# Optimization experiments

Measured on AMD Instinct MI355X. Metric: run time of the kernel, lower is better.

## Reference

```python
import jax, jax.numpy as jnp
import numpy as np

D = 15            # tree depth; leaves at level 0, root at level D
INPUT_DIM = 64
MEM_DIM = 256     # must equal 4*INPUT_DIM (h-update mixes rr with x)
HID_DIM = 128


def _lin(key, fi, fo):
    kw, kb = jax.random.split(key)
    w = jax.random.normal(kw, (fi, fo), jnp.float32) / np.sqrt(fi)
    b = jax.random.normal(kb, (fo,), jnp.float32) * 0.01
    return w, b


def setup_inputs() -> dict:
    key = jax.random.key(0)
    N = 2 ** (D + 1) - 1          # 65535 nodes (complete binary tree, heap order)
    I = 2 ** D - 1                # internal nodes
    depth = np.floor(np.log2(np.arange(1, N + 1))).astype(np.int64)  # depth of node i
    node_order_np = D - depth     # leaves -> 0, root -> D
    parents = np.repeat(np.arange(I, dtype=np.int64), 2)   # sorted, consecutive per parent
    children = np.arange(1, N, dtype=np.int64)             # heap children 2i+1, 2i+2
    adjacency_list = jnp.asarray(np.stack([parents, children], axis=1))
    edge_order = jnp.asarray(node_order_np[parents])
    ks = jax.random.split(key, 24)
    inp = {
        'oper_feat': jax.random.uniform(ks[0], (N, 4), jnp.float32),
        'tb_feat': jax.random.uniform(ks[1], (N, 11), jnp.float32),
        'filter_feat': jax.random.uniform(ks[2], (N, 18), jnp.float32),
        'join_feat': jax.random.uniform(ks[3], (N, 37), jnp.float32),
        'c_a': jax.random.normal(ks[4], (N, MEM_DIM), jnp.float32) * 0.1,
        'c_b': jax.random.normal(ks[5], (N, 5 * INPUT_DIM), jnp.float32) * 0.1,
    }
    inp['w_op1'], inp['b_op1'] = _lin(ks[6], 4, INPUT_DIM)
    inp['w_op2'], inp['b_op2'] = _lin(ks[7], INPUT_DIM, INPUT_DIM)
    inp['w_tb1'], inp['b_tb1'] = _lin(ks[8], 11, INPUT_DIM)
    inp['w_tb2'], inp['b_tb2'] = _lin(ks[9], INPUT_DIM, INPUT_DIM)
    inp['w_ft1'], inp['b_ft1'] = _lin(ks[10], 18, INPUT_DIM)
    inp['w_ft2'], inp['b_ft2'] = _lin(ks[11], INPUT_DIM, INPUT_DIM)
    inp['w_jn1'], inp['b_jn1'] = _lin(ks[12], 37, INPUT_DIM)
    inp['w_jn2'], inp['b_jn2'] = _lin(ks[13], INPUT_DIM, INPUT_DIM)
    inp['w_xou'], inp['b_xou'] = _lin(ks[14], 4 * INPUT_DIM, 3 * MEM_DIM)
    inp['w_ab'], inp['b_ab'] = _lin(ks[15], MEM_DIM, MEM_DIM)
    inp['w_btoa'], inp['b_btoa'] = _lin(ks[16], 5 * INPUT_DIM, MEM_DIM)
    inp['w_ca'], inp['b_ca'] = _lin(ks[17], 4 * INPUT_DIM, MEM_DIM)
    inp['w_cb'], inp['b_cb'] = _lin(ks[18], 4 * INPUT_DIM, MEM_DIM)
    inp['w_o1'], inp['b_o1'] = _lin(ks[19], MEM_DIM, HID_DIM)
    inp['w_o2'], inp['b_o2'] = _lin(ks[20], HID_DIM, 1)
    inp['node_order'] = jnp.asarray(node_order_np)
    inp['adjacency_list'] = adjacency_list
    inp['edge_order'] = edge_order
    inp['feed'] = 0
    return inp


def _mlp2(f, w1, b1, w2, b2):
    return jax.nn.relu(jax.nn.relu(f @ w1 + b1) @ w2 + b2)


def reference(oper_feat, tb_feat, filter_feat, join_feat, c_a, c_b,
              w_op1, b_op1, w_op2, b_op2, w_tb1, b_tb1, w_tb2, b_tb2,
              w_ft1, b_ft1, w_ft2, b_ft2, w_jn1, b_jn1, w_jn2, b_jn2,
              w_xou, b_xou, w_ab, b_ab, w_btoa, b_btoa, w_ca, b_ca,
              w_cb, b_cb, w_o1, b_o1, w_o2, b_o2,
              node_order, adjacency_list, edge_order, feed):
    N = node_order.shape[0]
    op = _mlp2(oper_feat, w_op1, b_op1, w_op2, b_op2)
    tb = _mlp2(tb_feat, w_tb1, b_tb1, w_tb2, b_tb2)
    ft = _mlp2(filter_feat, w_ft1, b_ft1, w_ft2, b_ft2)
    jn = _mlp2(join_feat, w_jn1, b_jn1, w_jn2, b_jn2)
    x = jnp.concatenate([op, tb, ft, jn], axis=1)        # [N, 4*input_dim] == [N, mem_dim]
    xou = x @ w_xou + b_xou                               # [N, 3*mem_dim]
    xx, ff, rr = jnp.split(xou, 3, axis=1)
    ff = jax.nn.sigmoid(ff)
    rr = jax.nn.sigmoid(rr)
    cb = c_b @ w_btoa + b_btoa                            # con_mpl_btoa (no activation)
    wa = jax.nn.sigmoid(c_a @ w_ca + b_ca)
    wb = jax.nn.sigmoid(cb @ w_cb + b_cb)
    c_ab = jax.nn.relu((wa * c_a + wb * cb) @ w_ab + b_ab)
    c = jnp.zeros((N, MEM_DIM), x.dtype)
    h = jnp.zeros((N, MEM_DIM), x.dtype)
    c = jnp.where((node_order == 0)[:, None], c_a, c)
    c = jnp.where((node_order == feed)[:, None], c_ab, c)
    par = adjacency_list[:, 0]
    chi = adjacency_list[:, 1]
    L = int(node_order.max())
    for n in range(feed + 1, L + 1):
        em = (edge_order == n).astype(x.dtype)[:, None]
        # segment-sum children cell states into their parents (level-n edges only)
        c_sum = jax.ops.segment_sum(c[chi] * em, par, num_segments=N)
        nm = (node_order == n)[:, None]
        c = jnp.where(nm, ff * c_sum + (1.0 - ff) * xx, c)
        h = jnp.where(nm, rr * jnp.tanh(c) + (1.0 - rr) * x, h)
    hid = jax.nn.relu(h @ w_o1 + b_o1)
    return jax.nn.sigmoid(hid @ w_o2 + b_o2)              # [N, 1]
```

## Files before the change

### kernel.cpp

```cpp
#include <hip/hip_runtime.h>
#include <cstdint>

#define I_NODES 32767
#define N_NODES 65535
#define NLEAF   32768

typedef float f32x4 __attribute__((ext_vector_type(4)));
typedef short bf16x8 __attribute__((ext_vector_type(8)));
typedef int   i32x4 __attribute__((ext_vector_type(4)));

__device__ __forceinline__ float sigmoidf_(float v) {
    return 1.0f / (1.0f + __expf(-v));
}
__device__ __forceinline__ float tanhf_(float v) {
    return 1.0f - 2.0f / (1.0f + __expf(2.0f * v));
}
__device__ __forceinline__ short f2bf(float f) {
    union { float f; unsigned u; } v; v.f = f;
    unsigned r = (v.u + 0x7FFF + ((v.u >> 16) & 1)) >> 16;
    return (short)r;
}
__device__ __forceinline__ float bf2f(short b) {
    union { float f; unsigned u; } v; v.u = ((unsigned)(unsigned short)b) << 16;
    return v.f;
}

__global__ __launch_bounds__(256) void prep_weights(
    const float* __restrict__ w_xou, const float* __restrict__ w_btoa,
    const float* __restrict__ w_ca,  const float* __restrict__ w_cb,
    const float* __restrict__ w_ab,  const float* __restrict__ w_o1,
    const float* __restrict__ w_op1, const float* __restrict__ w_tb1,
    const float* __restrict__ w_ft1, const float* __restrict__ w_jn1,
    const float* __restrict__ w_op2, const float* __restrict__ w_tb2,
    const float* __restrict__ w_ft2, const float* __restrict__ w_jn2,
    const float* __restrict__ b_op1, const float* __restrict__ b_tb1,
    const float* __restrict__ b_ft1, const float* __restrict__ b_jn1,
    const float* __restrict__ b_op2, const float* __restrict__ b_tb2,
    const float* __restrict__ b_ft2, const float* __restrict__ b_jn2,
    short* __restrict__ wT_xou, short* __restrict__ wT_btoa,
    short* __restrict__ wT_ca,  short* __restrict__ wT_cb,
    short* __restrict__ wT_ab,  short* __restrict__ wT_o1,
    short* __restrict__ W1T,    short* __restrict__ W2T,
    float* __restrict__ b1cat,  float* __restrict__ b2cat)
{
    int r = blockIdx.x * 256 + threadIdx.x;
    if (r < 196608) { wT_xou[r] = f2bf(w_xou[(size_t)(r % 256) * 768 + r / 256]); return; }
    r -= 196608;
    if (r < 81920)  { wT_btoa[r] = f2bf(w_btoa[(size_t)(r % 320) * 256 + r / 320]); return; }
    r -= 81920;
    if (r < 65536)  { wT_ca[r] = f2bf(w_ca[(size_t)(r % 256) * 256 + r / 256]); return; }
    r -= 65536;
    if (r < 65536)  { wT_cb[r] = f2bf(w_cb[(size_t)(r % 256) * 256 + r / 256]); return; }
    r -= 65536;
    if (r < 65536)  { wT_ab[r] = f2bf(w_ab[(size_t)(r % 256) * 256 + r / 256]); return; }
    r -= 65536;
    if (r < 32768)  { wT_o1[r] = f2bf(w_o1[(size_t)(r % 256) * 128 + r / 256]); return; }
    r -= 32768;
    if (r < 24576) {
        int j = r / 96, k = r % 96;
        int s = j >> 6, jj = j & 63;
        int off = (s == 0) ? 0 : (s == 1) ? 4 : (s == 2) ? 15 : 33;
        int Ks  = (s == 0) ? 4 : (s == 1) ? 11 : (s == 2) ? 18 : 37;
        const float* w = (s == 0) ? w_op1 : (s == 1) ? w_tb1 : (s == 2) ? w_ft1 : w_jn1;
        W1T[r] = (k >= off && k < off + Ks) ? f2bf(w[(k - off) * 64 + jj]) : (short)0;
        return;
    }
    r -= 24576;
    if (r < 65536) {
        int j = r >> 8, k = r & 255;
        int s = j >> 6, jj = j & 63;
        const float* w = (s == 0) ? w_op2 : (s == 1) ? w_tb2 : (s == 2) ? w_ft2 : w_jn2;
        W2T[r] = ((k >> 6) == s) ? f2bf(w[(k & 63) * 64 + jj]) : (short)0;
        return;
    }
    r -= 65536;
    if (r < 256) {
        int s = r >> 6, jj = r & 63;
        b1cat[r] = (s == 0) ? b_op1[jj] : (s == 1) ? b_tb1[jj] : (s == 2) ? b_ft1[jj] : b_jn1[jj];
        return;
    }
    r -= 256;
    if (r < 256) {
        int s = r >> 6, jj = r & 63;
        b2cat[r] = (s == 0) ? b_op2[jj] : (s == 1) ? b_tb2[jj] : (s == 2) ? b_ft2[jj] : b_jn2[jj];
    }
}

__global__ __launch_bounds__(256) void pack_feat(
    const float* __restrict__ oper, const float* __restrict__ tbf,
    const float* __restrict__ ftf,  const float* __restrict__ jnf,
    short* __restrict__ xfeat)
{
    int idx = blockIdx.x * 256 + threadIdx.x;
    int node = idx / 96, f = idx - node * 96;
    float v = 0.0f;
    if (node < I_NODES) {
        if (f < 4)       v = oper[node * 4 + f];
        else if (f < 15) v = tbf[node * 11 + (f - 4)];
        else if (f < 33) v = ftf[node * 18 + (f - 15)];
        else if (f < 70) v = jnf[node * 37 + (f - 33)];
    }
    xfeat[idx] = f2bf(v);
}

__global__ __launch_bounds__(256) void conv_leaf_kernel(
    const float* __restrict__ c_a, const float* __restrict__ c_b,
    short* __restrict__ ca_o, short* __restrict__ cb_o)
{
    size_t i = (size_t)blockIdx.x * 256 + threadIdx.x;
    if (i < (size_t)NLEAF * 256) ca_o[i] = f2bf(c_a[(size_t)I_NODES * 256 + i]);
    if (i < (size_t)NLEAF * 320) cb_o[i] = f2bf(c_b[(size_t)I_NODES * 320 + i]);
}

template <int ACT, int MODE>
__global__ __launch_bounds__(256) void gemm_mfma(
    const short* __restrict__ A, const short* __restrict__ Bt,
    const float* __restrict__ bias,
    float* __restrict__ fout0, const float* __restrict__ caf,
    float* __restrict__ fout1, float* __restrict__ fout2,
    short* __restrict__ bout,
    const short* __restrict__ e1, const short* __restrict__ e2,
    int M, int K, int Nn)
{
    __shared__ short Asl[128 * 40];
    __shared__ short Bsl[128 * 40];

    const int tid = threadIdx.x;
    const int bm = blockIdx.x * 128;
    const int bn = blockIdx.y * 128;
    const int wave = tid >> 6, lane = tid & 63;
    const int m = lane & 15, q = lane >> 4;
    const int rw = (wave & 1) * 64, cw = (wave >> 1) * 64;

    f32x4 acc[4][4] = {};

    for (int k0 = 0; k0 < K; k0 += 32) {
#pragma unroll
        for (int i = 0; i < 2; i++) {
            int id = tid + i * 256;
            int row = id >> 2, ch = id & 3;
            i32x4 va = *(const i32x4*)(A + (size_t)(bm + row) * K + k0 + ch * 8);
            *(i32x4*)&Asl[row * 40 + ch * 8] = va;
            i32x4 vb = *(const i32x4*)(Bt + (size_t)(bn + row) * K + k0 + ch * 8);
            *(i32x4*)&Bsl[row * 40 + ch * 8] = vb;
        }
        __syncthreads();

        bf16x8 bfrag[4];
#pragma unroll
        for (int ct = 0; ct < 4; ct++)
            bfrag[ct] = *(const bf16x8*)&Bsl[(cw + ct * 16 + m) * 40 + q * 8];
#pragma unroll
        for (int rt = 0; rt < 4; rt++) {
            bf16x8 afrag = *(const bf16x8*)&Asl[(rw + rt * 16 + m) * 40 + q * 8];
#pragma unroll
            for (int ct = 0; ct < 4; ct++)
                acc[rt][ct] = __builtin_amdgcn_mfma_f32_16x16x32_bf16(
                    afrag, bfrag[ct], acc[rt][ct], 0, 0, 0);
        }
        __syncthreads();
    }

#pragma unroll
    for (int rt = 0; rt < 4; rt++) {
#pragma unroll
        for (int ct = 0; ct < 4; ct++) {
            int col = bn + cw + ct * 16 + m;
            float bv = bias[col];
#pragma unroll
            for (int r = 0; r < 4; r++) {
                int row = bm + rw + rt * 16 + q * 4 + r;
                float v = acc[rt][ct][r] + bv;
                if (MODE == 0) {
                    if (ACT == 1) v = fmaxf(v, 0.0f);
                    else if (ACT == 2) v = sigmoidf_(v);
                    fout0[(size_t)row * Nn + col] = v;
                } else if (MODE == 1) {
                    int seg = col >> 8, cc = col & 255;
                    if (seg == 0)      fout0[(size_t)row * 256 + cc] = v;
                    else if (seg == 1) fout1[(size_t)row * 256 + cc] = sigmoidf_(v);
                    else               fout2[(size_t)row * 256 + cc] = sigmoidf_(v);
                } else if (MODE == 2) {
                    if (ACT == 1) v = fmaxf(v, 0.0f);
                    else if (ACT == 2) v = sigmoidf_(v);
                    bout[(size_t)row * Nn + col] = f2bf(v);
                } else {
                    size_t idx = (size_t)row * 256 + col;
                    float t = bf2f(e1[idx]) * caf[idx] + sigmoidf_(v) * bf2f(e2[idx]);
                    bout[idx] = f2bf(t);
                }
            }
        }
    }
}

__global__ __launch_bounds__(256) void level_kernel(
    float* __restrict__ c, const float* __restrict__ ff,
    const float* __restrict__ xx, const float* __restrict__ rr,
    const short* __restrict__ x, short* __restrict__ h,
    int start)
{
    size_t idx = (size_t)blockIdx.x * 256 + threadIdx.x;
    int p = start + (int)(idx >> 8);
    int j = (int)(idx & 255);
    size_t pr = (size_t)p * 256 + j;
    float cs = c[(size_t)(2 * p + 1) * 256 + j] + c[(size_t)(2 * p + 2) * 256 + j];
    float f = ff[pr];
    float cv = f * cs + (1.0f - f) * xx[pr];
    c[pr] = cv;
    float r = rr[pr];
    h[pr] = f2bf(r * tanhf_(cv) + (1.0f - r) * bf2f(x[pr]));
}

__global__ __launch_bounds__(1024) void small_levels_kernel(
    float* __restrict__ c, const float* __restrict__ ff,
    const float* __restrict__ xx, const float* __restrict__ rr,
    const short* __restrict__ x, short* __restrict__ h)
{
    const int tid = threadIdx.x;
    for (int n = 8; n <= 15; n++) {
        int d = 15 - n;
        int start = (1 << d) - 1;
        int total = (1 << d) * 256;
        for (int idx = tid; idx < total; idx += 1024) {
            int p = start + (idx >> 8);
            int j = idx & 255;
            size_t pr = (size_t)p * 256 + j;
            float cs = c[(size_t)(2 * p + 1) * 256 + j] + c[(size_t)(2 * p + 2) * 256 + j];
            float f = ff[pr];
            float cv = f * cs + (1.0f - f) * xx[pr];
            c[pr] = cv;
            float r = rr[pr];
            h[pr] = f2bf(r * tanhf_(cv) + (1.0f - r) * bf2f(x[pr]));
        }
        __syncthreads();
    }
}

__global__ __launch_bounds__(256) void out2_kernel(
    const short* __restrict__ hid, const float* __restrict__ w_o2,
    const float* __restrict__ b_o2, const float* __restrict__ b_o1,
    float* __restrict__ out)
{
    int wave = threadIdx.x >> 6;
    int lane = threadIdx.x & 63;
    int node = blockIdx.x * 4 + wave;
    if (node >= N_NODES) return;
    float h0, h1;
    if (node < I_NODES) {
        const short* hrow = hid + (size_t)node * 128;
        h0 = bf2f(hrow[lane]); h1 = bf2f(hrow[lane + 64]);
    } else {
        h0 = fmaxf(b_o1[lane], 0.0f); h1 = fmaxf(b_o1[lane + 64], 0.0f);
    }
    float p = h0 * w_o2[lane] + h1 * w_o2[lane + 64];
#pragma unroll
    for (int off = 32; off > 0; off >>= 1) p += __shfl_xor(p, off);
    if (lane == 0) out[node] = sigmoidf_(p + b_o2[0]);
}

extern "C" void kernel_launch(void* const* d_in, const int* in_sizes, int n_in,
                              void* d_out, int out_size, void* d_ws, size_t ws_size,
                              hipStream_t stream)
{
    const float* oper  = (const float*)d_in[0];
    const float* tbf   = (const float*)d_in[1];
    const float* ftf   = (const float*)d_in[2];
    const float* jnf   = (const float*)d_in[3];
    const float* c_a   = (const float*)d_in[4];
    const float* c_b   = (const float*)d_in[5];
    const float* w_op1 = (const float*)d_in[6],  *b_op1 = (const float*)d_in[7];
    const float* w_op2 = (const float*)d_in[8],  *b_op2 = (const float*)d_in[9];
    const float* w_tb1 = (const float*)d_in[10], *b_tb1 = (const float*)d_in[11];
    const float* w_tb2 = (const float*)d_in[12], *b_tb2 = (const float*)d_in[13];
    const float* w_ft1 = (const float*)d_in[14], *b_ft1 = (const float*)d_in[15];
    const float* w_ft2 = (const float*)d_in[16], *b_ft2 = (const float*)d_in[17];
    const float* w_jn1 = (const float*)d_in[18], *b_jn1 = (const float*)d_in[19];
    const float* w_jn2 = (const float*)d_in[20], *b_jn2 = (const float*)d_in[21];
    const float* w_xou = (const float*)d_in[22], *b_xou = (const float*)d_in[23];
    const float* w_ab  = (const float*)d_in[24], *b_ab  = (const float*)d_in[25];
    const float* w_btoa= (const float*)d_in[26], *b_btoa= (const float*)d_in[27];
    const float* w_ca  = (const float*)d_in[28], *b_ca  = (const float*)d_in[29];
    const float* w_cb  = (const float*)d_in[30], *b_cb  = (const float*)d_in[31];
    const float* w_o1  = (const float*)d_in[32], *b_o1  = (const float*)d_in[33];
    const float* w_o2  = (const float*)d_in[34], *b_o2  = (const float*)d_in[35];

    char* WS = (char*)d_ws;
    short* wT_xou  = (short*)WS;
    short* wT_btoa = wT_xou  + 196608;
    short* wT_ca   = wT_btoa + 81920;
    short* wT_cb   = wT_ca   + 65536;
    short* wT_ab   = wT_cb   + 65536;
    short* wT_o1   = wT_ab   + 65536;
    short* W1T     = wT_o1   + 32768;
    short* W2T     = W1T     + 24576;
    float* b1cat   = (float*)(W2T + 65536);
    float* b2cat   = b1cat + 256;
    const size_t MB = 1 << 20;
    const size_t OFF_XF   = 2 * MB;
    const size_t OFF_HE   = OFF_XF   + (size_t)32768 * 96 * 2;
    const size_t OFF_X    = OFF_HE   + (size_t)32768 * 256 * 2;
    const size_t OFF_XX   = OFF_X    + (size_t)32768 * 256 * 2;
    const size_t OFF_FF   = OFF_XX   + (size_t)32768 * 256 * 4;
    const size_t OFF_RR   = OFF_FF   + (size_t)32768 * 256 * 4;
    const size_t OFF_C    = OFF_RR   + (size_t)32768 * 256 * 4;
    const size_t OFF_CA   = OFF_C    + (size_t)65536 * 256 * 4;
    const size_t OFF_CBIN = OFF_CA   + (size_t)32768 * 256 * 2;
    const size_t OFF_CB   = OFF_CBIN + (size_t)32768 * 320 * 2;
    const size_t OFF_WA   = OFF_CB   + (size_t)32768 * 256 * 2;

    short* xfeat = (short*)(WS + OFF_XF);
    short* henc  = (short*)(WS + OFF_HE);
    short* x     = (short*)(WS + OFF_X);
    float* xx    = (float*)(WS + OFF_XX);
    float* ff    = (float*)(WS + OFF_FF);
    float* rr    = (float*)(WS + OFF_RR);
    float* c     = (float*)(WS + OFF_C);
    short* cal   = (short*)(WS + OFF_CA);
    short* cbin  = (short*)(WS + OFF_CBIN);
    short* cb    = (short*)(WS + OFF_CB);
    short* wa    = (short*)(WS + OFF_WA);
    short* h     = (short*)(WS + OFF_CA);
    short* hid   = (short*)(WS + OFF_CB);
    float* out   = (float*)d_out;
    const float* caf = c_a + (size_t)I_NODES * 256;

    prep_weights<<<(598528 + 255) / 256, 256, 0, stream>>>(
        w_xou, w_btoa, w_ca, w_cb, w_ab, w_o1,
        w_op1, w_tb1, w_ft1, w_jn1, w_op2, w_tb2, w_ft2, w_jn2,
        b_op1, b_tb1, b_ft1, b_jn1, b_op2, b_tb2, b_ft2, b_jn2,
        wT_xou, wT_btoa, wT_ca, wT_cb, wT_ab, wT_o1, W1T, W2T, b1cat, b2cat);
    pack_feat<<<(32768 * 96) / 256, 256, 0, stream>>>(oper, tbf, ftf, jnf, xfeat);
    conv_leaf_kernel<<<(NLEAF * 320 + 255) / 256, 256, 0, stream>>>(c_a, c_b, cal, cbin);

    gemm_mfma<1, 2><<<dim3(256, 2), 256, 0, stream>>>(
        xfeat, W1T, b1cat, nullptr, nullptr, nullptr, nullptr, henc, nullptr, nullptr,
        32768, 96, 256);
    gemm_mfma<1, 2><<<dim3(256, 2), 256, 0, stream>>>(
        henc, W2T, b2cat, nullptr, nullptr, nullptr, nullptr, x, nullptr, nullptr,
        32768, 256, 256);

    gemm_mfma<0, 1><<<dim3(256, 6), 256, 0, stream>>>(
        x, wT_xou, b_xou, xx, nullptr, ff, rr, nullptr, nullptr, nullptr,
        32768, 256, 768);

    gemm_mfma<0, 2><<<dim3(256, 2), 256, 0, stream>>>(
        cbin, wT_btoa, b_btoa, nullptr, nullptr, nullptr, nullptr, cb, nullptr, nullptr,
        32768, 320, 256);
    gemm_mfma<2, 2><<<dim3(256, 2), 256, 0, stream>>>(
        cal, wT_ca, b_ca, nullptr, nullptr, nullptr, nullptr, wa, nullptr, nullptr,
        32768, 256, 256);
    gemm_mfma<0, 3><<<dim3(256, 2), 256, 0, stream>>>(
        cb, wT_cb, b_cb, nullptr, caf, nullptr, nullptr, wa , wa, cb,
        32768, 256, 256);
    gemm_mfma<1, 0><<<dim3(256, 2), 256, 0, stream>>>(
        wa, wT_ab, b_ab, c + (size_t)I_NODES * 256, nullptr, nullptr, nullptr,
        nullptr, nullptr, nullptr, 32768, 256, 256);

    for (int n = 1; n <= 7; n++) {
        int d = 15 - n;
        int start = (1 << d) - 1;
        int count = 1 << d;
        level_kernel<<<count, 256, 0, stream>>>(c, ff, xx, rr, x, h, start);
    }
    small_levels_kernel<<<1, 1024, 0, stream>>>(c, ff, xx, rr, x, h);

    gemm_mfma<1, 2><<<dim3(256, 1), 256, 0, stream>>>(
        h, wT_o1, b_o1, nullptr, nullptr, nullptr, nullptr, hid, nullptr, nullptr,
        32768, 256, 128);
    out2_kernel<<<(N_NODES + 3) / 4, 256, 0, stream>>>(hid, w_o2, b_o2, b_o1, out);
}
```

Baseline: 510.9 us.

## Fuse prep kernels, convert leaf inputs in GEMM, persistent level kernel with grid barrier

Merges the weight prep, feature packing and leaf output computation into one launch. The leaf c_a/c_b bf16 conversion pass is removed: the GEMM now reads fp32 directly and converts while loading tiles, and the btoa and ca GEMMs share a single launch. The 15 tree levels run in one persistent kernel of 256 blocks synchronised by an atomic grid barrier, and the final MLP layer is folded into the o1 GEMM epilogue, so the hid buffer and out2 kernel disappear. This cuts launch count and intermediate traffic. The cost is a spin barrier that relies on all 256 blocks being co-resident, and small levels now spread across many blocks with a barrier between each.

```diff
diff --git a/kernel.cpp b/kernel.cpp
--- a/kernel.cpp
+++ b/kernel.cpp
@@ -25,7 +25,7 @@
     return v.f;
 }
 
-__global__ __launch_bounds__(256) void prep_weights(
+__global__ __launch_bounds__(256) void prep_all(
     const float* __restrict__ w_xou, const float* __restrict__ w_btoa,
     const float* __restrict__ w_ca,  const float* __restrict__ w_cb,
     const float* __restrict__ w_ab,  const float* __restrict__ w_o1,
@@ -37,11 +37,17 @@
     const float* __restrict__ b_ft1, const float* __restrict__ b_jn1,
     const float* __restrict__ b_op2, const float* __restrict__ b_tb2,
     const float* __restrict__ b_ft2, const float* __restrict__ b_jn2,
+    const float* __restrict__ oper,  const float* __restrict__ tbf,
+    const float* __restrict__ ftf,   const float* __restrict__ jnf,
+    const float* __restrict__ b_o1,  const float* __restrict__ w_o2,
+    const float* __restrict__ b_o2,
     short* __restrict__ wT_xou, short* __restrict__ wT_btoa,
     short* __restrict__ wT_ca,  short* __restrict__ wT_cb,
     short* __restrict__ wT_ab,  short* __restrict__ wT_o1,
     short* __restrict__ W1T,    short* __restrict__ W2T,
-    float* __restrict__ b1cat,  float* __restrict__ b2cat)
+    float* __restrict__ b1cat,  float* __restrict__ b2cat,
+    short* __restrict__ xfeat,  float* __restrict__ outv,
+    int* __restrict__ bar)
 {
     int r = blockIdx.x * 256 + threadIdx.x;
     if (r < 196608) { wT_xou[r] = f2bf(w_xou[(size_t)(r % 256) * 768 + r / 256]); return; }
@@ -83,48 +89,45 @@
     if (r < 256) {
         int s = r >> 6, jj = r & 63;
         b2cat[r] = (s == 0) ? b_op2[jj] : (s == 1) ? b_tb2[jj] : (s == 2) ? b_ft2[jj] : b_jn2[jj];
-    }
-}
-
-__global__ __launch_bounds__(256) void pack_feat(
-    const float* __restrict__ oper, const float* __restrict__ tbf,
-    const float* __restrict__ ftf,  const float* __restrict__ jnf,
-    short* __restrict__ xfeat)
-{
-    int idx = blockIdx.x * 256 + threadIdx.x;
-    int node = idx / 96, f = idx - node * 96;
-    float v = 0.0f;
-    if (node < I_NODES) {
-        if (f < 4)       v = oper[node * 4 + f];
-        else if (f < 15) v = tbf[node * 11 + (f - 4)];
-        else if (f < 33) v = ftf[node * 18 + (f - 15)];
-        else if (f < 70) v = jnf[node * 37 + (f - 33)];
-    }
-    xfeat[idx] = f2bf(v);
-}
-
-__global__ __launch_bounds__(256) void conv_leaf_kernel(
-    const float* __restrict__ c_a, const float* __restrict__ c_b,
-    short* __restrict__ ca_o, short* __restrict__ cb_o)
-{
-    size_t i = (size_t)blockIdx.x * 256 + threadIdx.x;
-    if (i < (size_t)NLEAF * 256) ca_o[i] = f2bf(c_a[(size_t)I_NODES * 256 + i]);
-    if (i < (size_t)NLEAF * 320) cb_o[i] = f2bf(c_b[(size_t)I_NODES * 320 + i]);
-}
-
-template <int ACT, int MODE>
-__global__ __launch_bounds__(256) void gemm_mfma(
-    const short* __restrict__ A, const short* __restrict__ Bt,
+        return;
+    }
+    r -= 256;
+    if (r < 3145728) {
+        int node = r / 96, f = r - node * 96;
+        float v = 0.0f;
+        if (node < I_NODES) {
+            if (f < 4)       v = oper[node * 4 + f];
+            else if (f < 15) v = tbf[node * 11 + (f - 4)];
+            else if (f < 33) v = ftf[node * 18 + (f - 15)];
+            else if (f < 70) v = jnf[node * 37 + (f - 33)];
+        }
+        xfeat[r] = f2bf(v);
+        return;
+    }
+    r -= 3145728;
+    if (r < 32768) {
+        float s = 0.0f;
+        for (int k = 0; k < 128; k++) s += fmaxf(b_o1[k], 0.0f) * w_o2[k];
+        outv[I_NODES + r] = sigmoidf_(s + b_o2[0]);
+        return;
+    }
+    r -= 32768;
+    if (r == 0) *bar = 0;
+}
+
+template <int ACT, int MODE, int ASRC>
+__device__ __forceinline__ void gemm_body(
+    short* Asl, short* Bsl,
+    const void* __restrict__ Araw, const short* __restrict__ Bt,
     const float* __restrict__ bias,
     float* __restrict__ fout0, const float* __restrict__ caf,
     float* __restrict__ fout1, float* __restrict__ fout2,
     short* __restrict__ bout,
     const short* __restrict__ e1, const short* __restrict__ e2,
-    int M, int K, int Nn)
-{
-    __shared__ short Asl[128 * 40];
-    __shared__ short Bsl[128 * 40];
-
+    const float* __restrict__ w_o2, const float* __restrict__ b_o2,
+    float* __restrict__ outv,
+    int K, int Nn)
+{
     const int tid = threadIdx.x;
     const int bm = blockIdx.x * 128;
     const int bn = blockIdx.y * 128;
@@ -139,8 +142,20 @@
         for (int i = 0; i < 2; i++) {
             int id = tid + i * 256;
             int row = id >> 2, ch = id & 3;
-            i32x4 va = *(const i32x4*)(A + (size_t)(bm + row) * K + k0 + ch * 8);
-            *(i32x4*)&Asl[row * 40 + ch * 8] = va;
+            if (ASRC == 0) {
+                const short* As = (const short*)Araw;
+                i32x4 va = *(const i32x4*)(As + (size_t)(bm + row) * K + k0 + ch * 8);
+                *(i32x4*)&Asl[row * 40 + ch * 8] = va;
+            } else {
+                const float* Af = (const float*)Araw;
+                const float* src = Af + (size_t)(bm + row) * K + k0 + ch * 8;
+                f32x4 a0 = *(const f32x4*)src;
+                f32x4 a1 = *(const f32x4*)(src + 4);
+                bf16x8 t;
+                t[0] = f2bf(a0[0]); t[1] = f2bf(a0[1]); t[2] = f2bf(a0[2]); t[3] = f2bf(a0[3]);
+                t[4] = f2bf(a1[0]); t[5] = f2bf(a1[1]); t[6] = f2bf(a1[2]); t[7] = f2bf(a1[3]);
+                *(bf16x8*)&Asl[row * 40 + ch * 8] = t;
+            }
             i32x4 vb = *(const i32x4*)(Bt + (size_t)(bn + row) * K + k0 + ch * 8);
             *(i32x4*)&Bsl[row * 40 + ch * 8] = vb;
         }
@@ -159,6 +174,48 @@
                     afrag, bfrag[ct], acc[rt][ct], 0, 0, 0);
         }
         __syncthreads();
+    }
+
+    if (MODE == 4) {
+        float part[4][4];
+#pragma unroll
+        for (int rt = 0; rt < 4; rt++)
+#pragma unroll
+            for (int r = 0; r < 4; r++) part[rt][r] = 0.0f;
+#pragma unroll
+        for (int ct = 0; ct < 4; ct++) {
+            int col = cw + ct * 16 + m;
+            float bv = bias[col];
+            float wv = w_o2[col];
+#pragma unroll
+            for (int rt = 0; rt < 4; rt++)
+#pragma unroll
+                for (int r = 0; r < 4; r++)
+                    part[rt][r] += fmaxf(acc[rt][ct][r] + bv, 0.0f) * wv;
+        }
+#pragma unroll
+        for (int rt = 0; rt < 4; rt++)
+#pragma unroll
+            for (int r = 0; r < 4; r++) {
+#pragma unroll
+                for (int off = 1; off < 16; off <<= 1)
+                    part[rt][r] += __shfl_xor(part[rt][r], off);
+            }
+        float* sred = (float*)Asl;
+        if (m == 0) {
+#pragma unroll
+            for (int rt = 0; rt < 4; rt++)
+#pragma unroll
+                for (int r = 0; r < 4; r++)
+                    sred[(rw + rt * 16 + q * 4 + r) * 2 + (cw >> 6)] = part[rt][r];
+        }
+        __syncthreads();
+        if (tid < 128) {
+            int g = bm + tid;
+            if (g < I_NODES)
+                outv[g] = sigmoidf_(sred[tid * 2] + sred[tid * 2 + 1] + b_o2[0]);
+        }
+        return;
     }
 
 #pragma unroll
@@ -194,35 +251,58 @@
     }
 }
 
-__global__ __launch_bounds__(256) void level_kernel(
+template <int ACT, int MODE, int ASRC>
+__global__ __launch_bounds__(256) void gemm_k(
+    const void* A, const short* Bt, const float* bias,
+    float* fout0, const float* caf, float* fout1, float* fout2,
+    short* bout, const short* e1, const short* e2,
+    const float* w_o2, const float* b_o2, float* outv,
+    int K, int Nn)
+{
+    __shared__ short Asl[128 * 40];
+    __shared__ short Bsl[128 * 40];
+    gemm_body<ACT, MODE, ASRC>(Asl, Bsl, A, Bt, bias, fout0, caf, fout1, fout2,
+                               bout, e1, e2, w_o2, b_o2, outv, K, Nn);
+}
+
+__global__ __launch_bounds__(256) void gemm_leafpair(
+    const float* cbl, const short* wT_btoa, const float* b_btoa, short* cb,
+    const float* cal, const short* wT_ca,   const float* b_ca,   short* wa)
+{
+    __shared__ short Asl[128 * 40];
+    __shared__ short Bsl[128 * 40];
+    if (blockIdx.z == 0)
+        gemm_body<0, 2, 1>(Asl, Bsl, cbl, wT_btoa, b_btoa,
+                           nullptr, nullptr, nullptr, nullptr, cb,
+                           nullptr, nullptr, nullptr, nullptr, nullptr, 320, 256);
+    else
+        gemm_body<2, 2, 1>(Asl, Bsl, cal, wT_ca, b_ca,
+                           nullptr, nullptr, nullptr, nullptr, wa,
+                           nullptr, nullptr, nullptr, nullptr, nullptr, 256, 256);
+}
+
+__device__ __forceinline__ void gbar(int* bar, int target)
+{
+    __syncthreads();
+    if (threadIdx.x == 0) {
+        __threadfence();
+        __hip_atomic_fetch_add(bar, 1, __ATOMIC_RELEASE, __HIP_MEMORY_SCOPE_AGENT);
+        while (__hip_atomic_load(bar, __ATOMIC_ACQUIRE, __HIP_MEMORY_SCOPE_AGENT) < target)
+            __builtin_amdgcn_s_sleep(2);
+    }
+    __syncthreads();
+}
+
+__global__ __launch_bounds__(1024, 4) void levels_fused(
     float* __restrict__ c, const float* __restrict__ ff,
     const float* __restrict__ xx, const float* __restrict__ rr,
-    const short* __restrict__ x, short* __restrict__ h,
-    int start)
-{
-    size_t idx = (size_t)blockIdx.x * 256 + threadIdx.x;
-    int p = start + (int)(idx >> 8);
-    int j = (int)(idx & 255);
-    size_t pr = (size_t)p * 256 + j;
-    float cs = c[(size_t)(2 * p + 1) * 256 + j] + c[(size_t)(2 * p + 2) * 256 + j];
-    float f = ff[pr];
-    float cv = f * cs + (1.0f - f) * xx[pr];
-    c[pr] = cv;
-    float r = rr[pr];
-    h[pr] = f2bf(r * tanhf_(cv) + (1.0f - r) * bf2f(x[pr]));
-}
-
-__global__ __launch_bounds__(1024) void small_levels_kernel(
-    float* __restrict__ c, const float* __restrict__ ff,
-    const float* __restrict__ xx, const float* __restrict__ rr,
-    const short* __restrict__ x, short* __restrict__ h)
-{
-    const int tid = threadIdx.x;
-    for (int n = 8; n <= 15; n++) {
+    const short* __restrict__ x, short* __restrict__ h, int* bar)
+{
+    for (int n = 1; n <= 15; n++) {
         int d = 15 - n;
         int start = (1 << d) - 1;
         int total = (1 << d) * 256;
-        for (int idx = tid; idx < total; idx += 1024) {
+        for (int idx = blockIdx.x * 1024 + threadIdx.x; idx < total; idx += 256 * 1024) {
             int p = start + (idx >> 8);
             int j = idx & 255;
             size_t pr = (size_t)p * 256 + j;
@@ -233,30 +313,8 @@
             float r = rr[pr];
             h[pr] = f2bf(r * tanhf_(cv) + (1.0f - r) * bf2f(x[pr]));
         }
-        __syncthreads();
-    }
-}
-
-__global__ __launch_bounds__(256) void out2_kernel(
-    const short* __restrict__ hid, const float* __restrict__ w_o2,
-    const float* __restrict__ b_o2, const float* __restrict__ b_o1,
-    float* __restrict__ out)
-{
-    int wave = threadIdx.x >> 6;
-    int lane = threadIdx.x & 63;
-    int node = blockIdx.x * 4 + wave;
-    if (node >= N_NODES) return;
-    float h0, h1;
-    if (node < I_NODES) {
-        const short* hrow = hid + (size_t)node * 128;
-        h0 = bf2f(hrow[lane]); h1 = bf2f(hrow[lane + 64]);
-    } else {
-        h0 = fmaxf(b_o1[lane], 0.0f); h1 = fmaxf(b_o1[lane + 64], 0.0f);
-    }
-    float p = h0 * w_o2[lane] + h1 * w_o2[lane + 64];
-#pragma unroll
-    for (int off = 32; off > 0; off >>= 1) p += __shfl_xor(p, off);
-    if (lane == 0) out[node] = sigmoidf_(p + b_o2[0]);
+        if (n < 15) gbar(bar, 256 * n);
+    }
 }
 
 extern "C" void kernel_launch(void* const* d_in, const int* in_sizes, int n_in,
@@ -296,6 +354,8 @@
     short* W2T     = W1T     + 24576;
     float* b1cat   = (float*)(W2T + 65536);
     float* b2cat   = b1cat + 256;
+    int*   bar     = (int*)(WS + 0x1F0000);
+
     const size_t MB = 1 << 20;
     const size_t OFF_XF   = 2 * MB;
     const size_t OFF_HE   = OFF_XF   + (size_t)32768 * 96 * 2;
@@ -304,9 +364,8 @@
     const size_t OFF_FF   = OFF_XX   + (size_t)32768 * 256 * 4;
     const size_t OFF_RR   = OFF_FF   + (size_t)32768 * 256 * 4;
     const size_t OFF_C    = OFF_RR   + (size_t)32768 * 256 * 4;
-    const size_t OFF_CA   = OFF_C    + (size_t)65536 * 256 * 4;
-    const size_t OFF_CBIN = OFF_CA   + (size_t)32768 * 256 * 2;
-    const size_t OFF_CB   = OFF_CBIN + (size_t)32768 * 320 * 2;
+    const size_t OFF_H    = OFF_C    + (size_t)65536 * 256 * 4;
+    const size_t OFF_CB   = OFF_H    + (size_t)32768 * 256 * 2;
     const size_t OFF_WA   = OFF_CB   + (size_t)32768 * 256 * 2;
 
     short* xfeat = (short*)(WS + OFF_XF);
@@ -316,57 +375,44 @@
     float* ff    = (float*)(WS + OFF_FF);
     float* rr    = (float*)(WS + OFF_RR);
     float* c     = (float*)(WS + OFF_C);
-    short* cal   = (short*)(WS + OFF_CA);
-    short* cbin  = (short*)(WS + OFF_CBIN);
+    short* h     = (short*)(WS + OFF_H);
     short* cb    = (short*)(WS + OFF_CB);
     short* wa    = (short*)(WS + OFF_WA);
-    short* h     = (short*)(WS + OFF_CA);
-    short* hid   = (short*)(WS + OFF_CB);
     float* out   = (float*)d_out;
     const float* caf = c_a + (size_t)I_NODES * 256;
-
-    prep_weights<<<(598528 + 255) / 256, 256, 0, stream>>>(
+    const float* cbl = c_b + (size_t)I_NODES * 320;
+
+    prep_all<<<14755, 256, 0, stream>>>(
         w_xou, w_btoa, w_ca, w_cb, w_ab, w_o1,
         w_op1, w_tb1, w_ft1, w_jn1, w_op2, w_tb2, w_ft2, w_jn2,
         b_op1, b_tb1, b_ft1, b_jn1, b_op2, b_tb2, b_ft2, b_jn2,
-        wT_xou, wT_btoa, wT_ca, wT_cb, wT_ab, wT_o1, W1T, W2T, b1cat, b2cat);
-    pack_feat<<<(32768 * 96) / 256, 256, 0, stream>>>(oper, tbf, ftf, jnf, xfeat);
-    conv_leaf_kernel<<<(NLEAF * 320 + 255) / 256, 256, 0, stream>>>(c_a, c_b, cal, cbin);
-
-    gemm_mfma<1, 2><<<dim3(256, 2), 256, 0, stream>>>(
-        xfeat, W1T, b1cat, nullptr, nullptr, nullptr, nullptr, henc, nullptr, nullptr,
-        32768, 96, 256);
-    gemm_mfma<1, 2><<<dim3(256, 2), 256, 0, stream>>>(
-        henc, W2T, b2cat, nullptr, nullptr, nullptr, nullptr, x, nullptr, nullptr,
-        32768, 256, 256);
-
-    gemm_mfma<0, 1><<<dim3(256, 6), 256, 0, stream>>>(
-        x, wT_xou, b_xou, xx, nullptr, ff, rr, nullptr, nullptr, nullptr,
-        32768, 256, 768);
-
-    gemm_mfma<0, 2><<<dim3(256, 2), 256, 0, stream>>>(
-        cbin, wT_btoa, b_btoa, nullptr, nullptr, nullptr, nullptr, cb, nullptr, nullptr,
-        32768, 320, 256);
-    gemm_mfma<2, 2><<<dim3(256, 2), 256, 0, stream>>>(
-        cal, wT_ca, b_ca, nullptr, nullptr, nullptr, nullptr, wa, nullptr, nullptr,
-        32768, 256, 256);
-    gemm_mfma<0, 3><<<dim3(256, 2), 256, 0, stream>>>(
-        cb, wT_cb, b_cb, nullptr, caf, nullptr, nullptr, wa , wa, cb,
-        32768, 256, 256);
-    gemm_mfma<1, 0><<<dim3(256, 2), 256, 0, stream>>>(
+        oper, tbf, ftf, jnf, b_o1, w_o2, b_o2,
+        wT_xou, wT_btoa, wT_ca, wT_cb, wT_ab, wT_o1, W1T, W2T, b1cat, b2cat,
+        xfeat, out, bar);
+
+    gemm_k<1, 2, 0><<<dim3(256, 2), 256, 0, stream>>>(
+        xfeat, W1T, b1cat, nullptr, nullptr, nullptr, nullptr, henc,
+        nullptr, nullptr, nullptr, nullptr, nullptr, 96, 256);
+    gemm_k<1, 2, 0><<<dim3(256, 2), 256, 0, stream>>>(
+        henc, W2T, b2cat, nullptr, nullptr, nullptr, nullptr, x,
+        nullptr, nullptr, nullptr, nullptr, nullptr, 256, 256);
+
+    gemm_k<0, 1, 0><<<dim3(256, 6), 256, 0, stream>>>(
+        x, wT_xou, b_xou, xx, nullptr, ff, rr, nullptr,
+        nullptr, nullptr, nullptr, nullptr, nullptr, 256, 768);
+
+    gemm_leafpair<<<dim3(256, 2, 2), 256, 0, stream>>>(
+        cbl, wT_btoa, b_btoa, cb, caf, wT_ca, b_ca, wa);
+    gemm_k<0, 3, 0><<<dim3(256, 2), 256, 0, stream>>>(
+        cb, wT_cb, b_cb, nullptr, caf, nullptr, nullptr, wa ,
+        wa, cb, nullptr, nullptr, nullptr, 256, 256);
+    gemm_k<1, 0, 0><<<dim3(256, 2), 256, 0, stream>>>(
         wa, wT_ab, b_ab, c + (size_t)I_NODES * 256, nullptr, nullptr, nullptr,
-        nullptr, nullptr, nullptr, 32768, 256, 256);
-
-    for (int n = 1; n <= 7; n++) {
-        int d = 15 - n;
-        int start = (1 << d) - 1;
-        int count = 1 << d;
-        level_kernel<<<count, 256, 0, stream>>>(c, ff, xx, rr, x, h, start);
-    }
-    small_levels_kernel<<<1, 1024, 0, stream>>>(c, ff, xx, rr, x, h);
-
-    gemm_mfma<1, 2><<<dim3(256, 1), 256, 0, stream>>>(
-        h, wT_o1, b_o1, nullptr, nullptr, nullptr, nullptr, hid, nullptr, nullptr,
-        32768, 256, 128);
-    out2_kernel<<<(N_NODES + 3) / 4, 256, 0, stream>>>(hid, w_o2, b_o2, b_o1, out);
-}
+        nullptr, nullptr, nullptr, nullptr, nullptr, nullptr, 256, 256);
+
+    levels_fused<<<256, 1024, 0, stream>>>(c, ff, xx, rr, x, h, bar);
+
+    gemm_k<1, 4, 0><<<dim3(256, 1), 256, 0, stream>>>(
+        h, wT_o1, b_o1, nullptr, nullptr, nullptr, nullptr, nullptr,
+        nullptr, nullptr, w_o2, b_o2, out, 256, 128);
+}
```

Result: slower. 689.3 us (+34.9%).
